# Performance work log

Measured on AMD Instinct MI355X. Metric: run time of the kernel, lower is better.

Reference implementation:

```python
import jax, jax.numpy as jnp
import numpy as np

MARGIN = 5.0


def setup_inputs() -> dict:
    key = jax.random.key(0)
    k1, k2, k3 = jax.random.split(key, 3)
    N, D = 8192, 4096
    recon_x = jax.random.normal(k1, (N, D), dtype=jnp.float32)
    x = jax.random.normal(k2, (N, D), dtype=jnp.float32)
    targets = jax.random.randint(k3, (N,), 0, 2, dtype=jnp.int64)
    return {"recon_x": recon_x, "x": x, "targets": targets}


def reference(recon_x, x, targets):
    # per-sample L2 distance between recon_x and x: [N]
    d = jnp.sqrt(jnp.sum((recon_x - x) ** 2, axis=1)) + 0.001
    pos = targets == 1  # anchor-positive samples -> dist_ap
    neg = targets == 0  # negative samples       -> dist_an
    # all pos-neg pairs: MarginRankingLoss(dist_an, dist_ap, y=1)
    #   = mean over pairs of max(0, dist_ap - dist_an + margin)
    pair_mask = pos[:, None] & neg[None, :]  # [N, N]
    elem = jnp.maximum(d[:, None] - d[None, :] + MARGIN, 0.0)
    cnt = jnp.sum(pair_mask).astype(elem.dtype)
    return jnp.sum(jnp.where(pair_mask, elem, 0.0)) / cnt
```

## Files before the change

### kernel.cpp

```cpp
#include <hip/hip_runtime.h>
#include <math.h>

#define N_ROWS 8192
#define D_COLS 4096
#define MARGIN 5.0f

__global__ void init_kernel(double* __restrict__ sum) { *sum = 0.0; }

__global__ __launch_bounds__(256) void dist_kernel(
    const float* __restrict__ rx, const float* __restrict__ x,
    const int* __restrict__ tgt, float* __restrict__ dp, float* __restrict__ dn) {
  const int row = blockIdx.x;
  const float4* a = reinterpret_cast<const float4*>(rx) + (size_t)row * (D_COLS / 4);
  const float4* b = reinterpret_cast<const float4*>(x)  + (size_t)row * (D_COLS / 4);
  float s = 0.f;
#pragma unroll
  for (int k = 0; k < D_COLS / 4 / 256; ++k) {
    float4 va = a[threadIdx.x + k * 256];
    float4 vb = b[threadIdx.x + k * 256];
    float d0 = va.x - vb.x, d1 = va.y - vb.y, d2 = va.z - vb.z, d3 = va.w - vb.w;
    s = fmaf(d0, d0, s); s = fmaf(d1, d1, s);
    s = fmaf(d2, d2, s); s = fmaf(d3, d3, s);
  }
#pragma unroll
  for (int off = 32; off; off >>= 1) s += __shfl_down(s, off, 64);
  __shared__ float ws[4];
  const int lane = threadIdx.x & 63, wid = threadIdx.x >> 6;
  if (lane == 0) ws[wid] = s;
  __syncthreads();
  if (threadIdx.x == 0) {
    float tot = ws[0] + ws[1] + ws[2] + ws[3];
    float dd = sqrtf(tot) + 0.001f;
    int t = tgt[row];
    dp[row] = (t == 1) ? dd : -INFINITY;
    dn[row] = (t == 0) ? dd : INFINITY;
  }
}

__global__ __launch_bounds__(256) void pair_kernel(
    const float* __restrict__ dp, const float* __restrict__ dn,
    double* __restrict__ sum) {
  float r[N_ROWS / 256];
#pragma unroll
  for (int k = 0; k < N_ROWS / 256; ++k) r[k] = dn[threadIdx.x + k * 256];
  float acc = 0.f;
  for (int i = blockIdx.x; i < N_ROWS; i += gridDim.x) {
    float dpi = dp[i];
    if (dpi == -INFINITY) continue;
    float dpi5 = dpi + MARGIN;
#pragma unroll
    for (int k = 0; k < N_ROWS / 256; ++k) acc += fmaxf(dpi5 - r[k], 0.f);
  }
#pragma unroll
  for (int off = 32; off; off >>= 1) acc += __shfl_down(acc, off, 64);
  __shared__ float ws[4];
  const int lane = threadIdx.x & 63, wid = threadIdx.x >> 6;
  if (lane == 0) ws[wid] = acc;
  __syncthreads();
  if (threadIdx.x == 0)
    atomicAdd(sum, (double)(ws[0] + ws[1] + ws[2] + ws[3]));
}

__global__ __launch_bounds__(256) void final_kernel(
    const int* __restrict__ tgt, const double* __restrict__ sum,
    float* __restrict__ out) {
  int c = 0;
#pragma unroll
  for (int k = 0; k < N_ROWS / 256; ++k) c += (tgt[threadIdx.x + k * 256] == 1);
#pragma unroll
  for (int off = 32; off; off >>= 1) c += __shfl_down(c, off, 64);
  __shared__ int ws[4];
  const int lane = threadIdx.x & 63, wid = threadIdx.x >> 6;
  if (lane == 0) ws[wid] = c;
  __syncthreads();
  if (threadIdx.x == 0) {
    long long np = ws[0] + ws[1] + ws[2] + ws[3];
    long long cnt = np * (long long)(N_ROWS - np);
    out[0] = (float)(*sum / (double)cnt);
  }
}

extern "C" void kernel_launch(void* const* d_in, const int* in_sizes, int n_in,
                              void* d_out, int out_size, void* d_ws, size_t ws_size,
                              hipStream_t stream) {
  const float* rx  = (const float*)d_in[0];
  const float* x   = (const float*)d_in[1];
  const int*   tgt = (const int*)d_in[2];
  float* out = (float*)d_out;

  float*  dp  = (float*)d_ws;
  float*  dn  = dp + N_ROWS;
  double* sum = (double*)(dn + N_ROWS);

  init_kernel<<<1, 1, 0, stream>>>(sum);
  dist_kernel<<<N_ROWS, 256, 0, stream>>>(rx, x, tgt, dp, dn);
  pair_kernel<<<1024, 256, 0, stream>>>(dp, dn, sum);
  final_kernel<<<1, 256, 0, stream>>>(tgt, sum, out);
}
```

Before: 289.3 us.

## Fold init and final kernels into dist/pair kernels with last-block ticket reduction

The separate init and final kernels are removed. Zeroing of the accumulators moves into the first block of the distance kernel, and the final division runs in the last pair block, chosen by an atomic ticket and a threadfence. Positive counts are gathered via atomicAdd while the pair loop runs. The distance kernel now gives each wavefront one row instead of each 256-thread block, which drops the shared-memory reduction and the block barrier. This cuts two kernel launches but relies on cross-block atomic ordering for correctness.

```diff
diff --git a/kernel.cpp b/kernel.cpp
--- a/kernel.cpp
+++ b/kernel.cpp
@@ -4,33 +4,30 @@
 #define N_ROWS 8192
 #define D_COLS 4096
 #define MARGIN 5.0f
-
-__global__ void init_kernel(double* __restrict__ sum) { *sum = 0.0; }
+#define PAIR_BLOCKS 1024
 
 __global__ __launch_bounds__(256) void dist_kernel(
     const float* __restrict__ rx, const float* __restrict__ x,
-    const int* __restrict__ tgt, float* __restrict__ dp, float* __restrict__ dn) {
-  const int row = blockIdx.x;
+    const int* __restrict__ tgt, float* __restrict__ dp, float* __restrict__ dn,
+    double* __restrict__ sum, int* __restrict__ ticket, int* __restrict__ npos) {
+  if (blockIdx.x == 0 && threadIdx.x == 0) { *sum = 0.0; *ticket = 0; *npos = 0; }
+  const int lane = threadIdx.x & 63;
+  const int row  = blockIdx.x * 4 + (threadIdx.x >> 6);
   const float4* a = reinterpret_cast<const float4*>(rx) + (size_t)row * (D_COLS / 4);
   const float4* b = reinterpret_cast<const float4*>(x)  + (size_t)row * (D_COLS / 4);
   float s = 0.f;
 #pragma unroll
-  for (int k = 0; k < D_COLS / 4 / 256; ++k) {
-    float4 va = a[threadIdx.x + k * 256];
-    float4 vb = b[threadIdx.x + k * 256];
+  for (int k = 0; k < D_COLS / 4 / 64; ++k) {
+    float4 va = a[lane + k * 64];
+    float4 vb = b[lane + k * 64];
     float d0 = va.x - vb.x, d1 = va.y - vb.y, d2 = va.z - vb.z, d3 = va.w - vb.w;
     s = fmaf(d0, d0, s); s = fmaf(d1, d1, s);
     s = fmaf(d2, d2, s); s = fmaf(d3, d3, s);
   }
 #pragma unroll
   for (int off = 32; off; off >>= 1) s += __shfl_down(s, off, 64);
-  __shared__ float ws[4];
-  const int lane = threadIdx.x & 63, wid = threadIdx.x >> 6;
-  if (lane == 0) ws[wid] = s;
-  __syncthreads();
-  if (threadIdx.x == 0) {
-    float tot = ws[0] + ws[1] + ws[2] + ws[3];
-    float dd = sqrtf(tot) + 0.001f;
+  if (lane == 0) {
+    float dd = sqrtf(s) + 0.001f;
     int t = tgt[row];
     dp[row] = (t == 1) ? dd : -INFINITY;
     dn[row] = (t == 0) ? dd : INFINITY;
@@ -39,14 +36,17 @@
 
 __global__ __launch_bounds__(256) void pair_kernel(
     const float* __restrict__ dp, const float* __restrict__ dn,
-    double* __restrict__ sum) {
+    double* __restrict__ sum, int* __restrict__ ticket, int* __restrict__ npos,
+    float* __restrict__ out) {
   float r[N_ROWS / 256];
 #pragma unroll
   for (int k = 0; k < N_ROWS / 256; ++k) r[k] = dn[threadIdx.x + k * 256];
   float acc = 0.f;
-  for (int i = blockIdx.x; i < N_ROWS; i += gridDim.x) {
+  int cnt = 0;
+  for (int i = blockIdx.x; i < N_ROWS; i += PAIR_BLOCKS) {
     float dpi = dp[i];
     if (dpi == -INFINITY) continue;
+    ++cnt;
     float dpi5 = dpi + MARGIN;
 #pragma unroll
     for (int k = 0; k < N_ROWS / 256; ++k) acc += fmaxf(dpi5 - r[k], 0.f);
@@ -57,26 +57,17 @@
   const int lane = threadIdx.x & 63, wid = threadIdx.x >> 6;
   if (lane == 0) ws[wid] = acc;
   __syncthreads();
-  if (threadIdx.x == 0)
+  if (threadIdx.x == 0) {
     atomicAdd(sum, (double)(ws[0] + ws[1] + ws[2] + ws[3]));
-}
-
-__global__ __launch_bounds__(256) void final_kernel(
-    const int* __restrict__ tgt, const double* __restrict__ sum,
-    float* __restrict__ out) {
-  int c = 0;
-#pragma unroll
-  for (int k = 0; k < N_ROWS / 256; ++k) c += (tgt[threadIdx.x + k * 256] == 1);
-#pragma unroll
-  for (int off = 32; off; off >>= 1) c += __shfl_down(c, off, 64);
-  __shared__ int ws[4];
-  const int lane = threadIdx.x & 63, wid = threadIdx.x >> 6;
-  if (lane == 0) ws[wid] = c;
-  __syncthreads();
-  if (threadIdx.x == 0) {
-    long long np = ws[0] + ws[1] + ws[2] + ws[3];
-    long long cnt = np * (long long)(N_ROWS - np);
-    out[0] = (float)(*sum / (double)cnt);
+    atomicAdd(npos, cnt);
+    __threadfence();
+    int t = atomicAdd(ticket, 1);
+    if (t == PAIR_BLOCKS - 1) {
+      double s = atomicAdd(sum, 0.0);
+      long long np = (long long)atomicAdd(npos, 0);
+      long long c = np * (long long)(N_ROWS - np);
+      out[0] = (float)(s / (double)c);
+    }
   }
 }
 
@@ -88,12 +79,12 @@
   const int*   tgt = (const int*)d_in[2];
   float* out = (float*)d_out;
 
-  float*  dp  = (float*)d_ws;
-  float*  dn  = dp + N_ROWS;
-  double* sum = (double*)(dn + N_ROWS);
+  float*  dp     = (float*)d_ws;
+  float*  dn     = dp + N_ROWS;
+  double* sum    = (double*)(dn + N_ROWS);
+  int*    ticket = (int*)(sum + 1);
+  int*    npos   = ticket + 1;
 
-  init_kernel<<<1, 1, 0, stream>>>(sum);
-  dist_kernel<<<N_ROWS, 256, 0, stream>>>(rx, x, tgt, dp, dn);
-  pair_kernel<<<1024, 256, 0, stream>>>(dp, dn, sum);
-  final_kernel<<<1, 256, 0, stream>>>(tgt, sum, out);
+  dist_kernel<<<N_ROWS / 4, 256, 0, stream>>>(rx, x, tgt, dp, dn, sum, ticket, npos);
+  pair_kernel<<<PAIR_BLOCKS, 256, 0, stream>>>(dp, dn, sum, ticket, npos, out);
 }
```

After: 315.3 us. 9.0% more time.
